# Optimization experiments

Measured on AMD Instinct MI355X. Metric: run time of the kernel, lower is better.

The kernel has to match this reference:

```python
import jax, jax.numpy as jnp
import numpy as np

EPS = 1e-5  # equinox LayerNorm default eps

def setup_inputs() -> dict:
    key = jax.random.key(0)
    k1, k2, k3, k4, k5 = jax.random.split(key, 5)
    heads, d, dH, N = 16, 1024, 64, 2048
    # lecun-normal-ish scaling for fan_in=d
    s = 1.0 / np.sqrt(d)
    return {
        "x": jax.random.normal(k1, (d, N), dtype=jnp.float32),
        "WQ": jax.random.normal(k2, (heads, d, dH), dtype=jnp.float32) * s,
        "WK": jax.random.normal(k3, (heads, d, dH), dtype=jnp.float32) * s,
        "WV": jax.random.normal(k4, (heads, d, dH), dtype=jnp.float32) * s,
        "W0": jax.random.normal(k5, (d, d), dtype=jnp.float32) * s,
    }

def reference(x, WQ, WK, WV, W0):
    # x: [d, N]
    residual = x
    # equinox LayerNorm over full shape (d, N), no affine params
    mean = jnp.mean(x)
    var = jnp.var(x)
    xn = (x - mean) * jax.lax.rsqrt(var + EPS)
    # project: [h, d_model, dH] x [d_model, N] -> [h, dH, N]
    Q = jnp.einsum('hcd,ci->hdi', WQ, xn)
    K = jnp.einsum('hcd,ci->hdi', WK, xn)
    V = jnp.einsum('hcd,ci->hdi', WV, xn)
    dH = WK.shape[-1]
    dot = jnp.einsum('hdi,hdj->hij', Q, K)  # [h, N, N]
    alpha = jax.nn.softmax(dot / jnp.sqrt(jnp.asarray(dH, dot.dtype)), axis=-1)
    attn = jnp.einsum('hij,hdj->hdi', alpha, V)  # [h, dH, N]
    N = attn.shape[2]
    attn = attn.reshape(-1, N)  # [d, N]
    out = W0 @ attn
    return out + residual
```

## Files before the change

kernel.cpp:

```cpp
#include <hip/hip_runtime.h>
#include <math.h>

typedef unsigned short u16;
typedef _Float16 f16;
typedef __attribute__((ext_vector_type(8))) short bf16x8;
typedef __attribute__((ext_vector_type(8))) unsigned short u16x8;
typedef __attribute__((ext_vector_type(4))) float f32x4;
typedef __attribute__((ext_vector_type(4))) f16 f16x4;

#define D_MODEL 1024
#define SEQ_N   2048
#define HEADS   16
#define DHEAD   64
#define M3      3072
#define JSPLIT  4
#define JCHUNK  (SEQ_N / JSPLIT)

#define GLOBAL_AS __attribute__((address_space(1)))
#define LDS_AS    __attribute__((address_space(3)))
#define ASYNC16(gp, lp) __builtin_amdgcn_global_load_lds( \
    (const GLOBAL_AS unsigned int*)(gp), (LDS_AS unsigned int*)(lp), 16, 0, 0)

__device__ __forceinline__ u16 f2bf(float f) {
  union { float f; unsigned int u; } v; v.f = f;
  unsigned int r = v.u + 0x7fffu + ((v.u >> 16) & 1u);
  return (u16)(r >> 16);
}

__global__ __launch_bounds__(256) void ln_reduce1(const float* __restrict__ x,
                                                  double* __restrict__ part, int n4) {
  const float4* x4 = (const float4*)x;
  double s = 0.0, ss = 0.0;
  for (int idx = blockIdx.x * blockDim.x + threadIdx.x; idx < n4;
       idx += gridDim.x * blockDim.x) {
    float4 v = x4[idx];
    s  += (double)v.x + (double)v.y + (double)v.z + (double)v.w;
    ss += (double)v.x * v.x + (double)v.y * v.y + (double)v.z * v.z + (double)v.w * v.w;
  }
  __shared__ double ls[256], lss[256];
  int t = threadIdx.x;
  ls[t] = s; lss[t] = ss;
  __syncthreads();
  for (int off = 128; off > 0; off >>= 1) {
    if (t < off) { ls[t] += ls[t + off]; lss[t] += lss[t + off]; }
    __syncthreads();
  }
  if (t == 0) { part[2 * blockIdx.x] = ls[0]; part[2 * blockIdx.x + 1] = lss[0]; }
}

__global__ __launch_bounds__(256) void ln_norm_t(const float* __restrict__ x,
                                                 const double* __restrict__ part,
                                                 u16* __restrict__ xnt) {
  __shared__ float tile[64][65];
  __shared__ float sstat[2];
  int t = threadIdx.x;
  {
    double* ls = (double*)&tile[0][0];
    double* lss = ls + 256;
    ls[t]  = part[2 * t] + part[2 * (t + 256)];
    lss[t] = part[2 * t + 1] + part[2 * (t + 256) + 1];
    __syncthreads();
    for (int off = 128; off > 0; off >>= 1) {
      if (t < off) { ls[t] += ls[t + off]; lss[t] += lss[t + off]; }
      __syncthreads();
    }
    if (t == 0) {
      double inv = 1.0 / ((double)D_MODEL * (double)SEQ_N);
      double mean = ls[0] * inv;
      double var  = lss[0] * inv - mean * mean;
      sstat[0] = (float)mean;
      sstat[1] = (float)(1.0 / sqrt(var + 1e-5));
    }
    __syncthreads();
  }
  float mean = sstat[0], rstd = sstat[1];
  int ib = blockIdx.x * 64, cb = blockIdx.y * 64;
  __syncthreads();
#pragma unroll
  for (int r = 0; r < 4; ++r) {
    int c = (t >> 4) + r * 16;
    int i4 = (t & 15) * 4;
    float4 v = *(const float4*)(&x[(size_t)(cb + c) * SEQ_N + ib + i4]);
    tile[c][i4 + 0] = (v.x - mean) * rstd;
    tile[c][i4 + 1] = (v.y - mean) * rstd;
    tile[c][i4 + 2] = (v.z - mean) * rstd;
    tile[c][i4 + 3] = (v.w - mean) * rstd;
  }
  __syncthreads();
#pragma unroll
  for (int r = 0; r < 2; ++r) {
    int i = (t >> 3) + r * 32;
    int c8 = (t & 7) * 8;
    u16x8 o;
#pragma unroll
    for (int j = 0; j < 8; ++j) o[j] = f2bf(tile[c8 + j][i]);
    *(u16x8*)(&xnt[(size_t)(ib + i) * D_MODEL + cb + c8]) = o;
  }
}

__global__ __launch_bounds__(256) void pack_qkv(const float* __restrict__ WQ,
                                                const float* __restrict__ WK,
                                                const float* __restrict__ WV,
                                                u16* __restrict__ Wp) {
  __shared__ float tile[32][65];
  const float* W = (blockIdx.z == 0) ? WQ : ((blockIdx.z == 1) ? WK : WV);
  int h = blockIdx.y, cb = blockIdx.x * 32;
  int t = threadIdx.x;
  int dh = t & 63, cl = t >> 6;
  for (int r = 0; r < 8; ++r) {
    int c = cl + r * 4;
    tile[c][dh] = W[((size_t)h * D_MODEL + cb + c) * DHEAD + dh];
  }
  __syncthreads();
  int c2 = t & 31, d2 = t >> 5;
  for (int r = 0; r < 8; ++r) {
    int dd = d2 + r * 8;
    Wp[(size_t)((blockIdx.z * HEADS + h) * DHEAD + dd) * D_MODEL + cb + c2] =
        f2bf(tile[c2][dd]);
  }
}

__global__ __launch_bounds__(256) void pack_w0(const float* __restrict__ W0,
                                               u16* __restrict__ W0p, int n4) {
  int idx = blockIdx.x * blockDim.x + threadIdx.x;
  if (idx >= n4) return;
  float4 v = ((const float4*)W0)[idx];
  unsigned int lo = (unsigned int)f2bf(v.x) | ((unsigned int)f2bf(v.y) << 16);
  unsigned int hi = (unsigned int)f2bf(v.z) | ((unsigned int)f2bf(v.w) << 16);
  uint2 o; o.x = lo; o.y = hi;
  *(uint2*)(&W0p[(size_t)idx * 4]) = o;
}

__global__ __launch_bounds__(256) void gemm_qkv(const u16* __restrict__ A,
                                                const u16* __restrict__ Bt,
                                                u16* __restrict__ Qt,
                                                u16* __restrict__ Kt,
                                                f16* __restrict__ Vb) {
  union SM {
    struct { u16 A[128 * 32]; u16 B[64 * 32]; } st;
    u16 qk[64][130];
    u16 v[128][66];
  };
  __shared__ __align__(16) SM sm;
  int t = threadIdx.x;
  int lane = t & 63, w = t >> 6;
  int g = lane >> 4, l16 = lane & 15;
  int b = blockIdx.x;
  int xcd = b & 7, s = b >> 3;
  int mt = xcd * 3 + (s % 3);
  int nt = s / 3;
  int mb = mt * 128, nb = nt * 64;

  f32x4 acc[2][4];
#pragma unroll
  for (int i = 0; i < 2; ++i)
#pragma unroll
    for (int j = 0; j < 4; ++j) acc[i][j] = (f32x4){0.f, 0.f, 0.f, 0.f};

  int srow = t >> 2, scol = (t & 3) * 8;
  const u16* Ag0 = A + (size_t)(mb + srow) * D_MODEL + scol;
  const u16* Ag1 = A + (size_t)(mb + 64 + srow) * D_MODEL + scol;
  const u16* Bg  = Bt + (size_t)(nb + srow) * D_MODEL + scol;

  for (int kb = 0; kb < D_MODEL; kb += 32) {
    ASYNC16(Ag0 + kb, &sm.st.A[t * 8]);
    ASYNC16(Ag1 + kb, &sm.st.A[2048 + t * 8]);
    ASYNC16(Bg + kb, &sm.st.B[t * 8]);
    __syncthreads();
    bf16x8 af[2], bf[4];
#pragma unroll
    for (int tm = 0; tm < 2; ++tm)
      af[tm] = *(const bf16x8*)(&sm.st.A[(w * 32 + tm * 16 + l16) * 32 + g * 8]);
#pragma unroll
    for (int tn = 0; tn < 4; ++tn)
      bf[tn] = *(const bf16x8*)(&sm.st.B[(tn * 16 + l16) * 32 + g * 8]);
#pragma unroll
    for (int tm = 0; tm < 2; ++tm)
#pragma unroll
      for (int tn = 0; tn < 4; ++tn)
        acc[tm][tn] = __builtin_amdgcn_mfma_f32_16x16x32_bf16(af[tm], bf[tn],
                                                              acc[tm][tn], 0, 0, 0);
    __syncthreads();
  }

  if (mb < 2 * D_MODEL) {
#pragma unroll
    for (int tm = 0; tm < 2; ++tm) {
      int m0 = w * 32 + tm * 16 + g * 4;
#pragma unroll
      for (int tn = 0; tn < 4; ++tn) {
        int nl = tn * 16 + l16;
        ushort4 o;
        o.x = f2bf(acc[tm][tn][0]); o.y = f2bf(acc[tm][tn][1]);
        o.z = f2bf(acc[tm][tn][2]); o.w = f2bf(acc[tm][tn][3]);
        *(ushort4*)(&sm.qk[nl][m0]) = o;
      }
    }
    __syncthreads();
    u16* T = (mb < D_MODEL) ? Qt : Kt;
    int mbase = (mb < D_MODEL) ? mb : mb - D_MODEL;
#pragma unroll
    for (int p = 0; p < 4; ++p) {
      int row = p * 16 + (t >> 4);
      int ch = (t & 15) * 8;
      *(uint4*)(&T[(size_t)(nb + row) * D_MODEL + mbase + ch]) =
          *(const uint4*)(&sm.qk[row][ch]);
    }
  } else {
#pragma unroll
    for (int tm = 0; tm < 2; ++tm) {
      int m0 = w * 32 + tm * 16 + g * 4;
#pragma unroll
      for (int tn = 0; tn < 4; ++tn) {
        int nl = tn * 16 + l16;
#pragma unroll
        for (int r = 0; r < 4; ++r)
          ((f16*)&sm.v[m0 + r][0])[nl] = (f16)acc[tm][tn][r];
      }
    }
    __syncthreads();
    int mbase = mb - 2 * D_MODEL;
#pragma unroll
    for (int p = 0; p < 4; ++p) {
      int row = p * 32 + (t >> 3);
      int ch = (t & 7) * 8;
      *(uint4*)(&Vb[(size_t)(mbase + row) * SEQ_N + nb + ch]) =
          *(const uint4*)(&sm.v[row][ch]);
    }
  }
}

__global__ __launch_bounds__(256) void gemm_bf16(const u16* __restrict__ A,
                                                 const u16* __restrict__ Bt,
                                                 float* __restrict__ C,
                                                 const float* __restrict__ res,
                                                 int M, int N, int K) {
  __shared__ __align__(16) u16 Alds[64 * 32];
  __shared__ __align__(16) u16 Blds[64 * 32];
  int t = threadIdx.x;
  int w = t >> 6, lane = t & 63;
  int g = lane >> 4, l16 = lane & 15;
  int b = blockIdx.x;
  int xcd = b & 7, s = b >> 3;
  int mpx = M / 512;
  int mt = xcd * mpx + (s % mpx);
  int nt = s / mpx;
  int mb = mt * 64, nb = nt * 64;
  f32x4 acc[4];
  for (int i = 0; i < 4; ++i) acc[i] = (f32x4){0.f, 0.f, 0.f, 0.f};
  int srow = t >> 2, scol = (t & 3) * 8;
  const u16* Ag = A + (size_t)(mb + srow) * K + scol;
  const u16* Bg = Bt + (size_t)(nb + srow) * K + scol;
  for (int kb = 0; kb < K; kb += 32) {
    ASYNC16(Ag + kb, &Alds[t * 8]);
    ASYNC16(Bg + kb, &Blds[t * 8]);
    __syncthreads();
    bf16x8 af = *(const bf16x8*)(&Alds[(w * 16 + l16) * 32 + g * 8]);
#pragma unroll
    for (int tn = 0; tn < 4; ++tn) {
      bf16x8 bf = *(const bf16x8*)(&Blds[(tn * 16 + l16) * 32 + g * 8]);
      acc[tn] = __builtin_amdgcn_mfma_f32_16x16x32_bf16(af, bf, acc[tn], 0, 0, 0);
    }
    __syncthreads();
  }
  int col0 = nb + l16;
  int row0 = mb + w * 16 + g * 4;
#pragma unroll
  for (int tn = 0; tn < 4; ++tn) {
    int col = col0 + tn * 16;
#pragma unroll
    for (int r = 0; r < 4; ++r) {
      int row = row0 + r;
      float v = acc[tn][r];
      if (res) v += res[(size_t)row * N + col];
      C[(size_t)row * N + col] = v;
    }
  }
}

__global__ __launch_bounds__(256, 8) void attn_mfma(const u16* __restrict__ Qt,
                                                    const u16* __restrict__ Kt,
                                                    const f16* __restrict__ Vb,
                                                    f16* __restrict__ Opart,
                                                    float* __restrict__ Lpart) {
  __shared__ __align__(16) u16 Klds[64][72];
  __shared__ __align__(16) f16 Vlds[64][72];
  int b = blockIdx.x;
  int xcd = b & 7, slot = b >> 3;
  int combo = xcd * 8 + (slot >> 5);
  int qt = slot & 31;
  int h = combo & 15;
  int sp = combo >> 4;
  int ib = qt * 64;
  int j0 = sp * JCHUNK;
  int t = threadIdx.x;
  int w = t >> 6, lane = t & 63;
  int g = lane >> 4, l16 = lane & 15;

  bf16x8 bq[2];
  {
    const u16* qb = Qt + (size_t)(ib + w * 16 + l16) * D_MODEL + h * DHEAD + g * 8;
    bq[0] = *(const bf16x8*)(qb);
    bq[1] = *(const bf16x8*)(qb + 32);
  }

  f32x4 acc_o[4];
#pragma unroll
  for (int i = 0; i < 4; ++i) acc_o[i] = (f32x4){0.f, 0.f, 0.f, 0.f};
  float lsum = 0.f;

  int srow = t >> 3, sch = (t & 7) * 8;
  for (int it = 0; it < JCHUNK / 64; ++it) {
    int jb = j0 + it * 64;
    uint4 kr0 = *(const uint4*)(&Kt[(size_t)(jb + srow) * D_MODEL + h * DHEAD + sch]);
    uint4 kr1 = *(const uint4*)(&Kt[(size_t)(jb + srow + 32) * D_MODEL + h * DHEAD + sch]);
    uint4 vr0 = *(const uint4*)(&Vb[(size_t)(h * DHEAD + srow) * SEQ_N + jb + sch]);
    uint4 vr1 = *(const uint4*)(&Vb[(size_t)(h * DHEAD + srow + 32) * SEQ_N + jb + sch]);
    *(uint4*)(&Klds[srow][sch]) = kr0;
    *(uint4*)(&Klds[srow + 32][sch]) = kr1;
    *(uint4*)(&Vlds[srow][sch]) = vr0;
    *(uint4*)(&Vlds[srow + 32][sch]) = vr1;
    __syncthreads();

    f32x4 s[4];
#pragma unroll
    for (int i = 0; i < 4; ++i) s[i] = (f32x4){0.f, 0.f, 0.f, 0.f};
#pragma unroll
    for (int kk = 0; kk < 2; ++kk)
#pragma unroll
      for (int tn = 0; tn < 4; ++tn) {
        bf16x8 ak = *(const bf16x8*)(&Klds[tn * 16 + l16][kk * 32 + g * 8]);
        s[tn] = __builtin_amdgcn_mfma_f32_16x16x32_bf16(ak, bq[kk], s[tn], 0, 0, 0);
      }
    f16x4 pf[4];
#pragma unroll
    for (int tn = 0; tn < 4; ++tn)
#pragma unroll
      for (int r = 0; r < 4; ++r) {
        float pv = exp2f(fmaf(s[tn][r], 0.18033688f, -5.7707801f));
        lsum += pv;
        pf[tn][r] = (f16)pv;
      }
#pragma unroll
    for (int tn = 0; tn < 4; ++tn)
#pragma unroll
      for (int td = 0; td < 4; ++td) {
        f16x4 bv = *(const f16x4*)(&Vlds[td * 16 + l16][tn * 16 + g * 4]);
        acc_o[td] =
            __builtin_amdgcn_mfma_f32_16x16x16f16(pf[tn], bv, acc_o[td], 0, 0, 0);
      }
    __syncthreads();
  }

  lsum += __shfl_xor(lsum, 16, 64);
  lsum += __shfl_xor(lsum, 32, 64);
  if (g == 0)
    Lpart[((size_t)sp * HEADS + h) * SEQ_N + ib + w * 16 + l16] = lsum;

#pragma unroll
  for (int td = 0; td < 4; ++td) {
    int dhl = td * 16 + l16;
#pragma unroll
    for (int r = 0; r < 4; ++r)
      Vlds[w * 16 + g * 4 + r][dhl] = (f16)acc_o[td][r];
  }
  __syncthreads();
#pragma unroll
  for (int p = 0; p < 2; ++p) {
    int row = p * 32 + (t >> 3);
    int ch = (t & 7) * 8;
    *(uint4*)(&Opart[((size_t)sp * SEQ_N + ib + row) * D_MODEL + h * DHEAD + ch]) =
        *(const uint4*)(&Vlds[row][ch]);
  }
}

__global__ __launch_bounds__(256) void attn_combine(const f16* __restrict__ Opart,
                                                    const float* __restrict__ Lpart,
                                                    u16* __restrict__ attnt) {
  int i = blockIdx.x;
  int c = threadIdx.x * 4;
  int h = c >> 6;
  float l = 0.f;
#pragma unroll
  for (int s = 0; s < JSPLIT; ++s) l += Lpart[((size_t)s * HEADS + h) * SEQ_N + i];
  float o[4] = {0.f, 0.f, 0.f, 0.f};
#pragma unroll
  for (int s = 0; s < JSPLIT; ++s) {
    f16x4 v = *(const f16x4*)(&Opart[((size_t)s * SEQ_N + i) * D_MODEL + c]);
#pragma unroll
    for (int r = 0; r < 4; ++r) o[r] += (float)v[r];
  }
  float inv = 1.0f / l;
  ushort4 ob;
  ob.x = f2bf(o[0] * inv); ob.y = f2bf(o[1] * inv);
  ob.z = f2bf(o[2] * inv); ob.w = f2bf(o[3] * inv);
  *(ushort4*)(&attnt[(size_t)i * D_MODEL + c]) = ob;
}

extern "C" void kernel_launch(void* const* d_in, const int* in_sizes, int n_in,
                              void* d_out, int out_size, void* d_ws, size_t ws_size,
                              hipStream_t stream) {
  const float* x  = (const float*)d_in[0];
  const float* WQ = (const float*)d_in[1];
  const float* WK = (const float*)d_in[2];
  const float* WV = (const float*)d_in[3];
  const float* W0 = (const float*)d_in[4];
  float* out = (float*)d_out;

  char* ws = (char*)d_ws;
  size_t off = 0;
  double* part  = (double*)(ws + off); off += 8192;
  u16*    xnt   = (u16*)(ws + off); off += (size_t)SEQ_N * D_MODEL * 2;
  u16*    Wp    = (u16*)(ws + off); off += (size_t)M3 * D_MODEL * 2;
  u16*    W0p   = (u16*)(ws + off); off += (size_t)D_MODEL * D_MODEL * 2;
  u16*    Qt    = (u16*)(ws + off); off += (size_t)SEQ_N * D_MODEL * 2;
  u16*    Kt    = (u16*)(ws + off); off += (size_t)SEQ_N * D_MODEL * 2;
  f16*    Vb    = (f16*)(ws + off); off += (size_t)D_MODEL * SEQ_N * 2;
  u16*    attnt = (u16*)(ws + off); off += (size_t)SEQ_N * D_MODEL * 2;
  f16*    Opart = (f16*)(ws + off); off += (size_t)JSPLIT * SEQ_N * D_MODEL * 2;
  float*  Lpart = (float*)(ws + off); off += (size_t)JSPLIT * HEADS * SEQ_N * 4;

  ln_reduce1<<<512, 256, 0, stream>>>(x, part, (D_MODEL * SEQ_N) / 4);
  ln_norm_t<<<dim3(SEQ_N / 64, D_MODEL / 64), 256, 0, stream>>>(x, part, xnt);
  pack_qkv<<<dim3(D_MODEL / 32, HEADS, 3), 256, 0, stream>>>(WQ, WK, WV, Wp);
  pack_w0<<<(D_MODEL * D_MODEL / 4 + 255) / 256, 256, 0, stream>>>(W0, W0p,
                                                                   D_MODEL * D_MODEL / 4);
  gemm_qkv<<<(M3 / 128) * (SEQ_N / 64), 256, 0, stream>>>(Wp, xnt, Qt, Kt, Vb);
  attn_mfma<<<2048, 256, 0, stream>>>(Qt, Kt, Vb, Opart, Lpart);
  attn_combine<<<SEQ_N, 256, 0, stream>>>(Opart, Lpart, attnt);
  gemm_bf16<<<(D_MODEL / 64) * (SEQ_N / 64), 256, 0, stream>>>(W0p, attnt, out, x,
                                                               D_MODEL, SEQ_N, D_MODEL);
}
```

Baseline: 183.4 us.

## Merge prep kernels and register-prefetch 128-wide K/V tiles in attention

The LayerNorm reduction, QKV weight packing and W0 packing move into one kernel that dispatches on block index, removing two launches and letting the three independent jobs run concurrently. The attention kernel now stages 128 keys per iteration and prefetches the next K/V tile into registers while computing on the current one, which halves the number of barrier rounds and hides global load latency. In exchange, LDS per block roughly doubles and the occupancy hint drops from 8 to 4 blocks, and the extra prefetch registers add pressure.

```diff
diff --git a/kernel.cpp b/kernel.cpp
--- a/kernel.cpp
+++ b/kernel.cpp
@@ -27,25 +27,61 @@
   return (u16)(r >> 16);
 }
 
-__global__ __launch_bounds__(256) void ln_reduce1(const float* __restrict__ x,
-                                                  double* __restrict__ part, int n4) {
-  const float4* x4 = (const float4*)x;
-  double s = 0.0, ss = 0.0;
-  for (int idx = blockIdx.x * blockDim.x + threadIdx.x; idx < n4;
-       idx += gridDim.x * blockDim.x) {
-    float4 v = x4[idx];
-    s  += (double)v.x + (double)v.y + (double)v.z + (double)v.w;
-    ss += (double)v.x * v.x + (double)v.y * v.y + (double)v.z * v.z + (double)v.w * v.w;
-  }
-  __shared__ double ls[256], lss[256];
+__global__ __launch_bounds__(256) void prep(const float* __restrict__ x,
+                                            const float* __restrict__ WQ,
+                                            const float* __restrict__ WK,
+                                            const float* __restrict__ WV,
+                                            const float* __restrict__ W0,
+                                            double* __restrict__ part,
+                                            u16* __restrict__ Wp,
+                                            u16* __restrict__ W0p) {
+  __shared__ __align__(16) char smem[8448];
+  int b = blockIdx.x;
   int t = threadIdx.x;
-  ls[t] = s; lss[t] = ss;
-  __syncthreads();
-  for (int off = 128; off > 0; off >>= 1) {
-    if (t < off) { ls[t] += ls[t + off]; lss[t] += lss[t + off]; }
-    __syncthreads();
-  }
-  if (t == 0) { part[2 * blockIdx.x] = ls[0]; part[2 * blockIdx.x + 1] = lss[0]; }
+  if (b < 512) {
+    const float4* x4 = (const float4*)x;
+    double s = 0.0, ss = 0.0;
+    int n4 = (D_MODEL * SEQ_N) / 4;
+    for (int idx = b * 256 + t; idx < n4; idx += 512 * 256) {
+      float4 v = x4[idx];
+      s  += (double)v.x + (double)v.y + (double)v.z + (double)v.w;
+      ss += (double)v.x * v.x + (double)v.y * v.y + (double)v.z * v.z + (double)v.w * v.w;
+    }
+    double* ls = (double*)smem;
+    double* lss = ls + 256;
+    ls[t] = s; lss[t] = ss;
+    __syncthreads();
+    for (int off = 128; off > 0; off >>= 1) {
+      if (t < off) { ls[t] += ls[t + off]; lss[t] += lss[t + off]; }
+      __syncthreads();
+    }
+    if (t == 0) { part[2 * b] = ls[0]; part[2 * b + 1] = lss[0]; }
+  } else if (b < 2048) {
+    int b2 = b - 512;
+    int z = b2 >> 9, rem = b2 & 511;
+    int h = rem >> 5, cb = (rem & 31) * 32;
+    const float* W = (z == 0) ? WQ : ((z == 1) ? WK : WV);
+    float (*tile)[65] = (float(*)[65])smem;
+    int dh = t & 63, cl = t >> 6;
+    for (int r = 0; r < 8; ++r) {
+      int c = cl + r * 4;
+      tile[c][dh] = W[((size_t)h * D_MODEL + cb + c) * DHEAD + dh];
+    }
+    __syncthreads();
+    int c2 = t & 31, d2 = t >> 5;
+    for (int r = 0; r < 8; ++r) {
+      int dd = d2 + r * 8;
+      Wp[(size_t)((z * HEADS + h) * DHEAD + dd) * D_MODEL + cb + c2] =
+          f2bf(tile[c2][dd]);
+    }
+  } else {
+    int idx = (b - 2048) * 256 + t;
+    float4 v = ((const float4*)W0)[idx];
+    unsigned int lo = (unsigned int)f2bf(v.x) | ((unsigned int)f2bf(v.y) << 16);
+    unsigned int hi = (unsigned int)f2bf(v.z) | ((unsigned int)f2bf(v.w) << 16);
+    uint2 o; o.x = lo; o.y = hi;
+    *(uint2*)(&W0p[(size_t)idx * 4]) = o;
+  }
 }
 
 __global__ __launch_bounds__(256) void ln_norm_t(const float* __restrict__ x,
@@ -96,39 +132,6 @@
     for (int j = 0; j < 8; ++j) o[j] = f2bf(tile[c8 + j][i]);
     *(u16x8*)(&xnt[(size_t)(ib + i) * D_MODEL + cb + c8]) = o;
   }
-}
-
-__global__ __launch_bounds__(256) void pack_qkv(const float* __restrict__ WQ,
-                                                const float* __restrict__ WK,
-                                                const float* __restrict__ WV,
-                                                u16* __restrict__ Wp) {
-  __shared__ float tile[32][65];
-  const float* W = (blockIdx.z == 0) ? WQ : ((blockIdx.z == 1) ? WK : WV);
-  int h = blockIdx.y, cb = blockIdx.x * 32;
-  int t = threadIdx.x;
-  int dh = t & 63, cl = t >> 6;
-  for (int r = 0; r < 8; ++r) {
-    int c = cl + r * 4;
-    tile[c][dh] = W[((size_t)h * D_MODEL + cb + c) * DHEAD + dh];
-  }
-  __syncthreads();
-  int c2 = t & 31, d2 = t >> 5;
-  for (int r = 0; r < 8; ++r) {
-    int dd = d2 + r * 8;
-    Wp[(size_t)((blockIdx.z * HEADS + h) * DHEAD + dd) * D_MODEL + cb + c2] =
-        f2bf(tile[c2][dd]);
-  }
-}
-
-__global__ __launch_bounds__(256) void pack_w0(const float* __restrict__ W0,
-                                               u16* __restrict__ W0p, int n4) {
-  int idx = blockIdx.x * blockDim.x + threadIdx.x;
-  if (idx >= n4) return;
-  float4 v = ((const float4*)W0)[idx];
-  unsigned int lo = (unsigned int)f2bf(v.x) | ((unsigned int)f2bf(v.y) << 16);
-  unsigned int hi = (unsigned int)f2bf(v.z) | ((unsigned int)f2bf(v.w) << 16);
-  uint2 o; o.x = lo; o.y = hi;
-  *(uint2*)(&W0p[(size_t)idx * 4]) = o;
 }
 
 __global__ __launch_bounds__(256) void gemm_qkv(const u16* __restrict__ A,
@@ -278,13 +281,13 @@
   }
 }
 
-__global__ __launch_bounds__(256, 8) void attn_mfma(const u16* __restrict__ Qt,
+__global__ __launch_bounds__(256, 4) void attn_mfma(const u16* __restrict__ Qt,
                                                     const u16* __restrict__ Kt,
                                                     const f16* __restrict__ Vb,
                                                     f16* __restrict__ Opart,
                                                     float* __restrict__ Lpart) {
-  __shared__ __align__(16) u16 Klds[64][72];
-  __shared__ __align__(16) f16 Vlds[64][72];
+  __shared__ __align__(16) u16 Klds[128][72];
+  __shared__ __align__(16) f16 Vlds[64][136];
   int b = blockIdx.x;
   int xcd = b & 7, slot = b >> 3;
   int combo = xcd * 8 + (slot >> 5);
@@ -309,47 +312,69 @@
   for (int i = 0; i < 4; ++i) acc_o[i] = (f32x4){0.f, 0.f, 0.f, 0.f};
   float lsum = 0.f;
 
-  int srow = t >> 3, sch = (t & 7) * 8;
-  for (int it = 0; it < JCHUNK / 64; ++it) {
-    int jb = j0 + it * 64;
-    uint4 kr0 = *(const uint4*)(&Kt[(size_t)(jb + srow) * D_MODEL + h * DHEAD + sch]);
-    uint4 kr1 = *(const uint4*)(&Kt[(size_t)(jb + srow + 32) * D_MODEL + h * DHEAD + sch]);
-    uint4 vr0 = *(const uint4*)(&Vb[(size_t)(h * DHEAD + srow) * SEQ_N + jb + sch]);
-    uint4 vr1 = *(const uint4*)(&Vb[(size_t)(h * DHEAD + srow + 32) * SEQ_N + jb + sch]);
-    *(uint4*)(&Klds[srow][sch]) = kr0;
-    *(uint4*)(&Klds[srow + 32][sch]) = kr1;
-    *(uint4*)(&Vlds[srow][sch]) = vr0;
-    *(uint4*)(&Vlds[srow + 32][sch]) = vr1;
-    __syncthreads();
-
-    f32x4 s[4];
-#pragma unroll
-    for (int i = 0; i < 4; ++i) s[i] = (f32x4){0.f, 0.f, 0.f, 0.f};
-#pragma unroll
-    for (int kk = 0; kk < 2; ++kk)
-#pragma unroll
-      for (int tn = 0; tn < 4; ++tn) {
-        bf16x8 ak = *(const bf16x8*)(&Klds[tn * 16 + l16][kk * 32 + g * 8]);
-        s[tn] = __builtin_amdgcn_mfma_f32_16x16x32_bf16(ak, bq[kk], s[tn], 0, 0, 0);
+  int krow = t >> 3, kch = (t & 7) * 8;
+  int vdh = t >> 4, vch = (t & 15) * 8;
+  uint4 kr[4], vr[4];
+#pragma unroll
+  for (int l = 0; l < 4; ++l) {
+    kr[l] = *(const uint4*)(&Kt[(size_t)(j0 + l * 32 + krow) * D_MODEL + h * DHEAD + kch]);
+    vr[l] = *(const uint4*)(&Vb[(size_t)(h * DHEAD + l * 16 + vdh) * SEQ_N + j0 + vch]);
+  }
+#pragma unroll
+  for (int l = 0; l < 4; ++l) {
+    *(uint4*)(&Klds[l * 32 + krow][kch]) = kr[l];
+    *(uint4*)(&Vlds[l * 16 + vdh][vch]) = vr[l];
+  }
+  __syncthreads();
+
+  for (int r = 0; r < JCHUNK / 128; ++r) {
+    if (r + 1 < JCHUNK / 128) {
+      int jb = j0 + (r + 1) * 128;
+#pragma unroll
+      for (int l = 0; l < 4; ++l) {
+        kr[l] = *(const uint4*)(&Kt[(size_t)(jb + l * 32 + krow) * D_MODEL + h * DHEAD + kch]);
+        vr[l] = *(const uint4*)(&Vb[(size_t)(h * DHEAD + l * 16 + vdh) * SEQ_N + jb + vch]);
       }
-    f16x4 pf[4];
-#pragma unroll
-    for (int tn = 0; tn < 4; ++tn)
-#pragma unroll
-      for (int r = 0; r < 4; ++r) {
-        float pv = exp2f(fmaf(s[tn][r], 0.18033688f, -5.7707801f));
-        lsum += pv;
-        pf[tn][r] = (f16)pv;
+    }
+#pragma unroll
+    for (int half = 0; half < 2; ++half) {
+      f32x4 s[4];
+#pragma unroll
+      for (int i = 0; i < 4; ++i) s[i] = (f32x4){0.f, 0.f, 0.f, 0.f};
+#pragma unroll
+      for (int kk = 0; kk < 2; ++kk)
+#pragma unroll
+        for (int tn = 0; tn < 4; ++tn) {
+          bf16x8 ak = *(const bf16x8*)(&Klds[half * 64 + tn * 16 + l16][kk * 32 + g * 8]);
+          s[tn] = __builtin_amdgcn_mfma_f32_16x16x32_bf16(ak, bq[kk], s[tn], 0, 0, 0);
+        }
+      f16x4 pf[4];
+#pragma unroll
+      for (int tn = 0; tn < 4; ++tn)
+#pragma unroll
+        for (int rr = 0; rr < 4; ++rr) {
+          float pv = exp2f(fmaf(s[tn][rr], 0.18033688f, -5.7707801f));
+          lsum += pv;
+          pf[tn][rr] = (f16)pv;
+        }
+#pragma unroll
+      for (int tn = 0; tn < 4; ++tn)
+#pragma unroll
+        for (int td = 0; td < 4; ++td) {
+          f16x4 bv = *(const f16x4*)(&Vlds[td * 16 + l16][half * 64 + tn * 16 + g * 4]);
+          acc_o[td] =
+              __builtin_amdgcn_mfma_f32_16x16x16f16(pf[tn], bv, acc_o[td], 0, 0, 0);
+        }
+    }
+    __syncthreads();
+    if (r + 1 < JCHUNK / 128) {
+#pragma unroll
+      for (int l = 0; l < 4; ++l) {
+        *(uint4*)(&Klds[l * 32 + krow][kch]) = kr[l];
+        *(uint4*)(&Vlds[l * 16 + vdh][vch]) = vr[l];
       }
-#pragma unroll
-    for (int tn = 0; tn < 4; ++tn)
-#pragma unroll
-      for (int td = 0; td < 4; ++td) {
-        f16x4 bv = *(const f16x4*)(&Vlds[td * 16 + l16][tn * 16 + g * 4]);
-        acc_o[td] =
-            __builtin_amdgcn_mfma_f32_16x16x16f16(pf[tn], bv, acc_o[td], 0, 0, 0);
-      }
-    __syncthreads();
+      __syncthreads();
+    }
   }
 
   lsum += __shfl_xor(lsum, 16, 64);
@@ -420,11 +445,8 @@
   f16*    Opart = (f16*)(ws + off); off += (size_t)JSPLIT * SEQ_N * D_MODEL * 2;
   float*  Lpart = (float*)(ws + off); off += (size_t)JSPLIT * HEADS * SEQ_N * 4;
 
-  ln_reduce1<<<512, 256, 0, stream>>>(x, part, (D_MODEL * SEQ_N) / 4);
+  prep<<<3072, 256, 0, stream>>>(x, WQ, WK, WV, W0, part, Wp, W0p);
   ln_norm_t<<<dim3(SEQ_N / 64, D_MODEL / 64), 256, 0, stream>>>(x, part, xnt);
-  pack_qkv<<<dim3(D_MODEL / 32, HEADS, 3), 256, 0, stream>>>(WQ, WK, WV, Wp);
-  pack_w0<<<(D_MODEL * D_MODEL / 4 + 255) / 256, 256, 0, stream>>>(W0, W0p,
-                                                                   D_MODEL * D_MODEL / 4);
   gemm_qkv<<<(M3 / 128) * (SEQ_N / 64), 256, 0, stream>>>(Wp, xnt, Qt, Kt, Vb);
   attn_mfma<<<2048, 256, 0, stream>>>(Qt, Kt, Vb, Opart, Lpart);
   attn_combine<<<SEQ_N, 256, 0, stream>>>(Opart, Lpart, attnt);
```

Result: slower. 212.4 us (+15.8%).
